# Kernel tuning notes

Hardware: AMD Instinct MI355X
Metric: run time of the kernel (lower is better)

## Reference

```python
import jax, jax.numpy as jnp
import numpy as np

NUM_EMBEDDINGS = 8192
EMBEDDING_DIM = 512
COMMITMENT_COST = 0.25
N_INPUTS = 32768


def setup_inputs() -> dict:
    key = jax.random.key(0)
    k1, k2 = jax.random.split(key)
    inputs = jax.random.normal(k1, (N_INPUTS, EMBEDDING_DIM), dtype=jnp.float32)
    weight = jax.random.normal(k2, (NUM_EMBEDDINGS, EMBEDDING_DIM), dtype=jnp.float32)
    return {"inputs": inputs, "weight": weight}


def reference(inputs, weight):
    # distances[n, k] = ||x_n||^2 + ||w_k||^2 - 2 x_n . w_k   -> [N, K]
    distances = (
        jnp.sum(inputs ** 2, axis=1, keepdims=True)
        + jnp.sum(weight ** 2, axis=1)
        - 2.0 * (inputs @ weight.T)
    )
    probs = jax.nn.softmax(-distances, axis=-1)            # [N, K]
    idx = jnp.argmin(distances, axis=1)                    # [N]
    quantized = weight[idx]                                # gather == one-hot @ weight

    e_latent_loss = jnp.mean((jax.lax.stop_gradient(quantized) - inputs) ** 2)
    q_latent_loss = jnp.mean((quantized - jax.lax.stop_gradient(inputs)) ** 2)
    loss = q_latent_loss + COMMITMENT_COST * e_latent_loss

    # straight-through estimator
    quantized_st = inputs + jax.lax.stop_gradient(quantized - inputs)

    # avg over one-hot encodings == normalized code histogram
    counts = jnp.bincount(idx, length=NUM_EMBEDDINGS).astype(inputs.dtype)
    avg_probs = counts / inputs.shape[0]
    perplexity = jnp.exp(-jnp.sum(avg_probs * jnp.log(avg_probs + 1e-10)))

    return (quantized_st, probs, loss, perplexity)
```

## Files before the change

### kernel.cpp

```cpp
#include <hip/hip_runtime.h>
#include <hip/hip_fp16.h>
#include <math.h>

#define N_ROWS 32768
#define K_CODES 8192
#define DIM 512

#define OUT_Q 0
#define OUT_P ((size_t)N_ROWS * DIM)
#define OUT_LOSS (OUT_P + (size_t)N_ROWS * K_CODES)
#define OUT_PERP (OUT_LOSS + 1)

#define WS_WSQ 0
#define WS_CNT (K_CODES)
#define WS_ERR (2 * K_CODES)
#define WS_RED (2 * K_CODES + N_ROWS)
#define WS_F16 (2 * K_CODES + N_ROWS + 64)

#define XH_OFF ((size_t)0)
#define XL_OFF ((size_t)N_ROWS * DIM)
#define WH_OFF ((size_t)2 * N_ROWS * DIM)
#define WL_OFF ((size_t)2 * N_ROWS * DIM + (size_t)K_CODES * DIM)
#define F16_COUNT ((size_t)2 * (N_ROWS + K_CODES) * DIM)
#define WS_NEEDED ((size_t)WS_F16 * 4 + F16_COUNT * 2)

typedef _Float16 f16x8 __attribute__((ext_vector_type(8)));
typedef float f32x4 __attribute__((ext_vector_type(4)));

__device__ inline void load_lds16(const void* g, void* l) {
    __builtin_amdgcn_global_load_lds((const __attribute__((address_space(1))) void*)g,
                                     (__attribute__((address_space(3))) void*)l,
                                     16, 0, 0);
}

__device__ inline unsigned int fkey(float f) {
    unsigned int b = __float_as_uint(f);
    return b ^ ((unsigned int)((int)b >> 31) | 0x80000000u);
}
__device__ inline float fkey_inv(unsigned int k) {
    unsigned int b = (k & 0x80000000u) ? (k ^ 0x80000000u) : ~k;
    return __uint_as_float(b);
}

__global__ void wsq_kernel(const float* __restrict__ W, float* __restrict__ ws) {
    int row = blockIdx.x;
    int lane = threadIdx.x;
    const float* src = W + (size_t)row * DIM;
    float4 v0 = *(const float4*)(src + lane * 8);
    float4 v1 = *(const float4*)(src + lane * 8 + 4);
    float s = v0.x * v0.x + v0.y * v0.y + v0.z * v0.z + v0.w * v0.w
            + v1.x * v1.x + v1.y * v1.y + v1.z * v1.z + v1.w * v1.w;
#pragma unroll
    for (int off = 32; off > 0; off >>= 1) s += __shfl_down(s, off, 64);
    if (lane == 0) ws[WS_WSQ + row] = s;
}

__global__ void __launch_bounds__(256) convert_split_kernel(
    const float* __restrict__ X, const float* __restrict__ W,
    _Float16* __restrict__ f16base, float* __restrict__ ws) {
    const size_t NX8 = (size_t)N_ROWS * DIM / 8;
    size_t t = (size_t)blockIdx.x * 256 + threadIdx.x;
    const float* src;
    _Float16 *hd, *ld;
    bool isW = (t >= NX8);
    if (!isW) {
        src = X + t * 8;
        hd = f16base + XH_OFF + t * 8;
        ld = f16base + XL_OFF + t * 8;
    } else {
        size_t u = t - NX8;
        src = W + u * 8;
        hd = f16base + WH_OFF + u * 8;
        ld = f16base + WL_OFF + u * 8;
    }
    float4 v0 = *(const float4*)src;
    float4 v1 = *(const float4*)(src + 4);
    float v[8] = {v0.x, v0.y, v0.z, v0.w, v1.x, v1.y, v1.z, v1.w};
    f16x8 h, l;
    float s = 0.f;
#pragma unroll
    for (int i = 0; i < 8; ++i) {
        _Float16 hv = (_Float16)v[i];
        h[i] = hv;
        l[i] = (_Float16)(v[i] - (float)hv);
        s += v[i] * v[i];
    }
    *(f16x8*)hd = h;
    *(f16x8*)ld = l;
    if (isW) {
#pragma unroll
        for (int off = 32; off > 0; off >>= 1) s += __shfl_down(s, off, 64);
        if ((threadIdx.x & 63) == 0) ws[WS_WSQ + ((t - NX8) >> 6)] = s;
    }
}

#define LDSB 24576
#define AH_O 0
#define AL_O 8192
#define BH_O 16384
#define BL_O 20480

__global__ void __launch_bounds__(512, 2) gemm_dist_mfma_kernel(
    const _Float16* __restrict__ f16base, const float* __restrict__ ws,
    float* __restrict__ out) {
    __shared__ _Float16 lds[3 * LDSB];

    const int tid = threadIdx.x;
    const int w = tid >> 6;
    const int lane = tid & 63;

    int lin = blockIdx.y * 64 + blockIdx.x;
    int xcd = lin & 7;
    int idx = lin >> 3;
    const int bn = (xcd * 8 + (idx & 7)) * 128;
    const int bm = (idx >> 3) * 256;

    const int wr = w >> 1;
    const int wc = w & 1;
    const int q = lane >> 4;
    const int fm = lane & 15;
    const int l4 = lane >> 2;
    const int p = lane & 3;

    f32x4 acc[4][4];
#pragma unroll
    for (int i = 0; i < 4; ++i)
#pragma unroll
        for (int j = 0; j < 4; ++j) acc[i][j] = (f32x4){0.f, 0.f, 0.f, 0.f};

    auto stage = [&](int ks, _Float16* buf, int part) {
        const int kk = ks * 32;
        int g = w * 2 + part;
        int arow = g * 16 + l4;
        int ca = p ^ ((arow >> 1) & 3);
        size_t aoff = (size_t)(bm + arow) * DIM + kk + ca * 8;
        load_lds16(f16base + XH_OFF + aoff, buf + AH_O + g * 512);
        load_lds16(f16base + XL_OFF + aoff, buf + AL_O + g * 512);
        int brow = w * 16 + l4;
        int cb = p ^ ((brow >> 1) & 3);
        size_t boff = (size_t)(bn + brow) * DIM + kk + cb * 8;
        if (part == 0)
            load_lds16(f16base + WH_OFF + boff, buf + BH_O + w * 512);
        else
            load_lds16(f16base + WL_OFF + boff, buf + BL_O + w * 512);
    };

    _Float16* c0 = lds;
    _Float16* c1 = lds + LDSB;
    _Float16* c2 = lds + 2 * LDSB;

    stage(0, c0, 0); stage(0, c0, 1);
    stage(1, c1, 0); stage(1, c1, 1);
    asm volatile("s_waitcnt vmcnt(6)" ::: "memory");
    __builtin_amdgcn_s_barrier();
    __builtin_amdgcn_sched_barrier(0);

#pragma unroll 1
    for (int ks = 0; ks < 16; ++ks) {
        if (ks < 14) { stage(ks + 2, c2, 0); stage(ks + 2, c2, 1); }

        f16x8 bhv[4], blv[4], ahv[4], alv[4];
#pragma unroll
        for (int j = 0; j < 4; ++j) {
            int bb = wc * 64 + j * 16 + fm;
            int off = bb * 32 + ((q ^ ((bb >> 1) & 3)) * 8);
            bhv[j] = *(const f16x8*)&c0[BH_O + off];
            blv[j] = *(const f16x8*)&c0[BL_O + off];
        }
#pragma unroll
        for (int i = 0; i < 4; ++i) {
            int am = wr * 64 + i * 16 + fm;
            int off = am * 32 + ((q ^ ((am >> 1) & 3)) * 8);
            ahv[i] = *(const f16x8*)&c0[AH_O + off];
            alv[i] = *(const f16x8*)&c0[AL_O + off];
        }

        __builtin_amdgcn_s_setprio(1);
#pragma unroll
        for (int i = 0; i < 4; ++i)
#pragma unroll
            for (int j = 0; j < 4; ++j) {
                acc[i][j] = __builtin_amdgcn_mfma_f32_16x16x32_f16(
                    ahv[i], bhv[j], acc[i][j], 0, 0, 0);
                acc[i][j] = __builtin_amdgcn_mfma_f32_16x16x32_f16(
                    ahv[i], blv[j], acc[i][j], 0, 0, 0);
                acc[i][j] = __builtin_amdgcn_mfma_f32_16x16x32_f16(
                    alv[i], bhv[j], acc[i][j], 0, 0, 0);
            }
        __builtin_amdgcn_s_setprio(0);

        if (ks < 14) {
            asm volatile("s_waitcnt vmcnt(6)" ::: "memory");
        } else if (ks == 14) {
            asm volatile("s_waitcnt vmcnt(0)" ::: "memory");
        }
        __builtin_amdgcn_s_barrier();
        __builtin_amdgcn_sched_barrier(0);

        _Float16* t0 = c0; c0 = c1; c1 = c2; c2 = t0;
    }

    const float* wsq = ws + WS_WSQ;
    float* Dout = out + OUT_P;
    const int q4 = q * 4;
#pragma unroll
    for (int i = 0; i < 4; ++i) {
#pragma unroll
        for (int j = 0; j < 4; ++j) {
            int n = bn + wc * 64 + j * 16 + fm;
            float wn = wsq[n];
#pragma unroll
            for (int r = 0; r < 4; ++r) {
                int m = bm + wr * 64 + i * 16 + q4 + r;
                Dout[(size_t)m * K_CODES + n] = wn - 2.f * acc[i][j][r];
            }
        }
    }
}

#define BM 128
#define BN 128
#define BK 16

__global__ void __launch_bounds__(256) gemm_dist_fp32_kernel(
    const float* __restrict__ X, const float* __restrict__ W,
    const float* __restrict__ ws, float* __restrict__ out) {
    __shared__ float As[BK][BM];
    __shared__ float Bs[BK][BN];

    const int bn = blockIdx.x * BN;
    const int bm = blockIdx.y * BM;
    const int tid = threadIdx.x;
    const int tx = tid & 15;
    const int ty = tid >> 4;
    const int lr = tid >> 1;
    const int lc = (tid & 1) * 8;

    float acc[8][8];
#pragma unroll
    for (int i = 0; i < 8; ++i)
#pragma unroll
        for (int j = 0; j < 8; ++j) acc[i][j] = 0.f;

    const float* aptr = X + (size_t)(bm + lr) * DIM + lc;
    const float* bptr = W + (size_t)(bn + lr) * DIM + lc;

    for (int k0 = 0; k0 < DIM; k0 += BK) {
        float4 a0 = *(const float4*)(aptr + k0);
        float4 a1 = *(const float4*)(aptr + k0 + 4);
        float4 b0 = *(const float4*)(bptr + k0);
        float4 b1 = *(const float4*)(bptr + k0 + 4);
        __syncthreads();
        As[lc + 0][lr] = a0.x; As[lc + 1][lr] = a0.y;
        As[lc + 2][lr] = a0.z; As[lc + 3][lr] = a0.w;
        As[lc + 4][lr] = a1.x; As[lc + 5][lr] = a1.y;
        As[lc + 6][lr] = a1.z; As[lc + 7][lr] = a1.w;
        Bs[lc + 0][lr] = b0.x; Bs[lc + 1][lr] = b0.y;
        Bs[lc + 2][lr] = b0.z; Bs[lc + 3][lr] = b0.w;
        Bs[lc + 4][lr] = b1.x; Bs[lc + 5][lr] = b1.y;
        Bs[lc + 6][lr] = b1.z; Bs[lc + 7][lr] = b1.w;
        __syncthreads();
#pragma unroll
        for (int kk = 0; kk < BK; ++kk) {
            float a[8], b[8];
            *(float4*)&a[0] = *(const float4*)&As[kk][ty * 8];
            *(float4*)&a[4] = *(const float4*)&As[kk][ty * 8 + 4];
            *(float4*)&b[0] = *(const float4*)&Bs[kk][tx * 8];
            *(float4*)&b[4] = *(const float4*)&Bs[kk][tx * 8 + 4];
#pragma unroll
            for (int i = 0; i < 8; ++i)
#pragma unroll
                for (int j = 0; j < 8; ++j)
                    acc[i][j] = fmaf(a[i], b[j], acc[i][j]);
        }
    }

    const float* wsq = ws + WS_WSQ;
    const int m0 = bm + ty * 8;
    const int n0 = bn + tx * 8;
    float wn[8];
    *(float4*)&wn[0] = *(const float4*)(wsq + n0);
    *(float4*)&wn[4] = *(const float4*)(wsq + n0 + 4);
    float* Dout = out + OUT_P;
#pragma unroll
    for (int i = 0; i < 8; ++i) {
        float4 o0, o1;
        o0.x = wn[0] - 2.f * acc[i][0];
        o0.y = wn[1] - 2.f * acc[i][1];
        o0.z = wn[2] - 2.f * acc[i][2];
        o0.w = wn[3] - 2.f * acc[i][3];
        o1.x = wn[4] - 2.f * acc[i][4];
        o1.y = wn[5] - 2.f * acc[i][5];
        o1.z = wn[6] - 2.f * acc[i][6];
        o1.w = wn[7] - 2.f * acc[i][7];
        float* drow = Dout + (size_t)(m0 + i) * K_CODES + n0;
        *(float4*)(drow) = o0;
        *(float4*)(drow + 4) = o1;
    }
}

__global__ void __launch_bounds__(512) probs_quant_kernel(
    const float* __restrict__ X, const float* __restrict__ W,
    float* __restrict__ out, float* __restrict__ ws) {
    const int n = blockIdx.x;
    const int tid = threadIdx.x;
    __shared__ unsigned long long mred[8];
    __shared__ float fred[8];

    float4* Drow4 = (float4*)(out + OUT_P + (size_t)n * K_CODES);

    const float x = X[(size_t)n * DIM + tid];

    float4 e[4];
    unsigned long long best = ~0ull;
#pragma unroll
    for (int t = 0; t < 4; ++t) {
        float4 v = Drow4[tid + t * 512];
        e[t] = v;
        unsigned int c0 = (unsigned int)((tid + t * 512) * 4);
        unsigned long long k;
        k = ((unsigned long long)fkey(v.x) << 32) | (c0 + 0u);
        best = k < best ? k : best;
        k = ((unsigned long long)fkey(v.y) << 32) | (c0 + 1u);
        best = k < best ? k : best;
        k = ((unsigned long long)fkey(v.z) << 32) | (c0 + 2u);
        best = k < best ? k : best;
        k = ((unsigned long long)fkey(v.w) << 32) | (c0 + 3u);
        best = k < best ? k : best;
    }
#pragma unroll
    for (int d = 1; d < 64; d <<= 1) {
        unsigned long long o = __shfl_xor(best, d, 64);
        best = o < best ? o : best;
    }
    if ((tid & 63) == 0) mred[tid >> 6] = best;
    __syncthreads();
    unsigned long long bm = mred[0];
#pragma unroll
    for (int i = 1; i < 8; ++i) bm = mred[i] < bm ? mred[i] : bm;
    const float smin = fkey_inv((unsigned int)(bm >> 32));
    const int amin = (int)(bm & 0xFFFFFFFFu);

    float sum = 0.f;
#pragma unroll
    for (int t = 0; t < 4; ++t) {
        float4 v = e[t];
        float4 ev;
        ev.x = __expf(smin - v.x);
        ev.y = __expf(smin - v.y);
        ev.z = __expf(smin - v.z);
        ev.w = __expf(smin - v.w);
        e[t] = ev;
        sum += ev.x + ev.y + ev.z + ev.w;
    }
#pragma unroll
    for (int off = 32; off > 0; off >>= 1) sum += __shfl_down(sum, off, 64);
    if ((tid & 63) == 0) fred[tid >> 6] = sum;
    __syncthreads();
    float tot = fred[0];
#pragma unroll
    for (int i = 1; i < 8; ++i) tot += fred[i];
    const float inv = 1.0f / tot;

#pragma unroll
    for (int t = 0; t < 4; ++t) {
        float4 ev = e[t];
        ev.x *= inv; ev.y *= inv; ev.z *= inv; ev.w *= inv;
        Drow4[tid + t * 512] = ev;
    }

    const float qv = W[(size_t)amin * DIM + tid];
    out[OUT_Q + (size_t)n * DIM + tid] = qv;
    float d2 = qv - x;
    float err = d2 * d2;
#pragma unroll
    for (int off = 32; off > 0; off >>= 1) err += __shfl_down(err, off, 64);
    __syncthreads();
    if ((tid & 63) == 0) fred[tid >> 6] = err;
    __syncthreads();
    if (tid == 0) {
        float e8 = fred[0];
#pragma unroll
        for (int i = 1; i < 8; ++i) e8 += fred[i];
        ws[WS_ERR + n] = e8;
        atomicAdd(ws + WS_CNT + amin, 1.0f);
    }
}

__global__ void __launch_bounds__(256) finalize_part_kernel(
    float* __restrict__ ws) {
    __shared__ float red[256];
    const int b = blockIdx.x;
    const int tid = threadIdx.x;

    float errsum = 0.f;
    const int ebase = b * 1024;
#pragma unroll
    for (int j = tid; j < 1024; j += 256) errsum += ws[WS_ERR + ebase + j];

    float p = ws[WS_CNT + b * 256 + tid] * (1.0f / (float)N_ROWS);
    float ent = -p * logf(p + 1e-10f);

    red[tid] = errsum;
    __syncthreads();
    for (int st = 128; st > 0; st >>= 1) {
        if (tid < st) red[tid] += red[tid + st];
        __syncthreads();
    }
    if (tid == 0) ws[WS_RED + b] = red[0];
    __syncthreads();
    red[tid] = ent;
    __syncthreads();
    for (int st = 128; st > 0; st >>= 1) {
        if (tid < st) red[tid] += red[tid + st];
        __syncthreads();
    }
    if (tid == 0) ws[WS_RED + 32 + b] = red[0];
}

__global__ void __launch_bounds__(64) finalize_fin_kernel(
    float* __restrict__ out, const float* __restrict__ ws) {
    const int tid = threadIdx.x;
    float ev = tid < 32 ? ws[WS_RED + tid] : 0.f;
    float nv = tid < 32 ? ws[WS_RED + 32 + tid] : 0.f;
#pragma unroll
    for (int off = 32; off > 0; off >>= 1) {
        ev += __shfl_down(ev, off, 64);
        nv += __shfl_down(nv, off, 64);
    }
    if (tid == 0) {
        float mse = ev * (1.0f / ((float)N_ROWS * (float)DIM));
        out[OUT_LOSS] = mse + 0.25f * mse;
        out[OUT_PERP] = expf(nv);
    }
}

extern "C" void kernel_launch(void* const* d_in, const int* in_sizes, int n_in,
                              void* d_out, int out_size, void* d_ws, size_t ws_size,
                              hipStream_t stream) {
    const float* X = (const float*)d_in[0];
    const float* W = (const float*)d_in[1];
    float* out = (float*)d_out;
    float* ws = (float*)d_ws;

    hipMemsetAsync(ws + WS_CNT, 0, K_CODES * sizeof(float), stream);

    if (ws_size >= WS_NEEDED) {
        _Float16* f16base = (_Float16*)(ws + WS_F16);
        const int conv_blocks =
            (int)(((size_t)(N_ROWS + K_CODES) * DIM / 8 + 255) / 256);
        convert_split_kernel<<<conv_blocks, 256, 0, stream>>>(X, W, f16base, ws);

        dim3 ggrid(64, 128);
        gemm_dist_mfma_kernel<<<ggrid, 512, 0, stream>>>(f16base, ws, out);
    } else {
        wsq_kernel<<<K_CODES, 64, 0, stream>>>(W, ws);
        dim3 ggrid(K_CODES / BN, N_ROWS / BM);
        gemm_dist_fp32_kernel<<<ggrid, 256, 0, stream>>>(X, W, ws, out);
    }

    probs_quant_kernel<<<N_ROWS, 512, 0, stream>>>(X, W, out, ws);
    finalize_part_kernel<<<32, 256, 0, stream>>>(ws);
    finalize_fin_kernel<<<1, 64, 0, stream>>>(out, ws);
}
```

Before: 2.349 ms.

## Fuse per-tile softmax max/sum and argmin into GEMM epilogue, add combine pass

```diff
diff --git a/kernel.cpp b/kernel.cpp
--- a/kernel.cpp
+++ b/kernel.cpp
@@ -15,17 +15,23 @@
 #define WS_CNT (K_CODES)
 #define WS_ERR (2 * K_CODES)
 #define WS_RED (2 * K_CODES + N_ROWS)
-#define WS_F16 (2 * K_CODES + N_ROWS + 64)
+#define WS_ROWMI (WS_RED + 64)
+#define WS_PSUM (WS_ROWMI + 2 * N_ROWS)
+#define WS_PMIN (WS_PSUM + (size_t)N_ROWS * 64)
+#define WS_F16_FULL (WS_PMIN + (size_t)2 * N_ROWS * 64)
+#define WS_F16_LEG  (WS_RED + 64)
 
 #define XH_OFF ((size_t)0)
 #define XL_OFF ((size_t)N_ROWS * DIM)
 #define WH_OFF ((size_t)2 * N_ROWS * DIM)
 #define WL_OFF ((size_t)2 * N_ROWS * DIM + (size_t)K_CODES * DIM)
 #define F16_COUNT ((size_t)2 * (N_ROWS + K_CODES) * DIM)
-#define WS_NEEDED ((size_t)WS_F16 * 4 + F16_COUNT * 2)
+#define NEEDED_FULL ((size_t)WS_F16_FULL * 4 + F16_COUNT * 2)
+#define NEEDED_LEG  ((size_t)WS_F16_LEG * 4 + F16_COUNT * 2)
 
 typedef _Float16 f16x8 __attribute__((ext_vector_type(8)));
 typedef float f32x4 __attribute__((ext_vector_type(4)));
+typedef unsigned long long u64;
 
 __device__ inline void load_lds16(const void* g, void* l) {
     __builtin_amdgcn_global_load_lds((const __attribute__((address_space(1))) void*)g,
@@ -102,8 +108,9 @@
 
 __global__ void __launch_bounds__(512, 2) gemm_dist_mfma_kernel(
     const _Float16* __restrict__ f16base, const float* __restrict__ ws,
-    float* __restrict__ out) {
-    __shared__ _Float16 lds[3 * LDSB];
+    float* __restrict__ out, u64* __restrict__ pmin_g,
+    float* __restrict__ psum_g) {
+    __shared__ __align__(16) _Float16 lds[3 * LDSB];
 
     const int tid = threadIdx.x;
     const int w = tid >> 6;
@@ -114,6 +121,7 @@
     int idx = lin >> 3;
     const int bn = (xcd * 8 + (idx & 7)) * 128;
     const int bm = (idx >> 3) * 256;
+    const int tile = bn >> 7;
 
     const int wr = w >> 1;
     const int wc = w & 1;
@@ -157,9 +165,7 @@
 
 #pragma unroll 1
     for (int ks = 0; ks < 16; ++ks) {
-        if (ks < 14) { stage(ks + 2, c2, 0); stage(ks + 2, c2, 1); }
-
-        f16x8 bhv[4], blv[4], ahv[4], alv[4];
+        f16x8 bhv[4], blv[4];
 #pragma unroll
         for (int j = 0; j < 4; ++j) {
             int bb = wc * 64 + j * 16 + fm;
@@ -167,28 +173,51 @@
             bhv[j] = *(const f16x8*)&c0[BH_O + off];
             blv[j] = *(const f16x8*)&c0[BL_O + off];
         }
-#pragma unroll
-        for (int i = 0; i < 4; ++i) {
+        f16x8 ah[2], al[2];
+#pragma unroll
+        for (int i = 0; i < 2; ++i) {
             int am = wr * 64 + i * 16 + fm;
             int off = am * 32 + ((q ^ ((am >> 1) & 3)) * 8);
-            ahv[i] = *(const f16x8*)&c0[AH_O + off];
-            alv[i] = *(const f16x8*)&c0[AL_O + off];
-        }
-
+            ah[i] = *(const f16x8*)&c0[AH_O + off];
+            al[i] = *(const f16x8*)&c0[AL_O + off];
+        }
+        if (ks < 14) stage(ks + 2, c2, 0);
         __builtin_amdgcn_s_setprio(1);
 #pragma unroll
-        for (int i = 0; i < 4; ++i)
+        for (int i = 0; i < 2; ++i)
 #pragma unroll
             for (int j = 0; j < 4; ++j) {
                 acc[i][j] = __builtin_amdgcn_mfma_f32_16x16x32_f16(
-                    ahv[i], bhv[j], acc[i][j], 0, 0, 0);
+                    ah[i], bhv[j], acc[i][j], 0, 0, 0);
                 acc[i][j] = __builtin_amdgcn_mfma_f32_16x16x32_f16(
-                    ahv[i], blv[j], acc[i][j], 0, 0, 0);
+                    ah[i], blv[j], acc[i][j], 0, 0, 0);
                 acc[i][j] = __builtin_amdgcn_mfma_f32_16x16x32_f16(
-                    alv[i], bhv[j], acc[i][j], 0, 0, 0);
+                    al[i], bhv[j], acc[i][j], 0, 0, 0);
             }
         __builtin_amdgcn_s_setprio(0);
-
+        __builtin_amdgcn_s_barrier();
+
+#pragma unroll
+        for (int i = 0; i < 2; ++i) {
+            int am = wr * 64 + (i + 2) * 16 + fm;
+            int off = am * 32 + ((q ^ ((am >> 1) & 3)) * 8);
+            ah[i] = *(const f16x8*)&c0[AH_O + off];
+            al[i] = *(const f16x8*)&c0[AL_O + off];
+        }
+        if (ks < 14) stage(ks + 2, c2, 1);
+        __builtin_amdgcn_s_setprio(1);
+#pragma unroll
+        for (int i = 0; i < 2; ++i)
+#pragma unroll
+            for (int j = 0; j < 4; ++j) {
+                acc[i + 2][j] = __builtin_amdgcn_mfma_f32_16x16x32_f16(
+                    ah[i], bhv[j], acc[i + 2][j], 0, 0, 0);
+                acc[i + 2][j] = __builtin_amdgcn_mfma_f32_16x16x32_f16(
+                    ah[i], blv[j], acc[i + 2][j], 0, 0, 0);
+                acc[i + 2][j] = __builtin_amdgcn_mfma_f32_16x16x32_f16(
+                    al[i], bhv[j], acc[i + 2][j], 0, 0, 0);
+            }
+        __builtin_amdgcn_s_setprio(0);
         if (ks < 14) {
             asm volatile("s_waitcnt vmcnt(6)" ::: "memory");
         } else if (ks == 14) {
@@ -203,18 +232,145 @@
     const float* wsq = ws + WS_WSQ;
     float* Dout = out + OUT_P;
     const int q4 = q * 4;
+    float wnj[4];
+#pragma unroll
+    for (int j = 0; j < 4; ++j) wnj[j] = wsq[bn + wc * 64 + j * 16 + fm];
+
 #pragma unroll
     for (int i = 0; i < 4; ++i) {
 #pragma unroll
         for (int j = 0; j < 4; ++j) {
             int n = bn + wc * 64 + j * 16 + fm;
-            float wn = wsq[n];
 #pragma unroll
             for (int r = 0; r < 4; ++r) {
                 int m = bm + wr * 64 + i * 16 + q4 + r;
-                Dout[(size_t)m * K_CODES + n] = wn - 2.f * acc[i][j][r];
+                Dout[(size_t)m * K_CODES + n] = wnj[j] - 2.f * acc[i][j][r];
             }
         }
+    }
+
+    if (pmin_g) {
+        u64* hmin = (u64*)lds;
+        float* hsum = (float*)(hmin + 512);
+
+#pragma unroll
+        for (int i = 0; i < 4; ++i) {
+#pragma unroll
+            for (int r = 0; r < 4; ++r) {
+                u64 bk = ~0ull;
+#pragma unroll
+                for (int j = 0; j < 4; ++j) {
+                    float S = wnj[j] - 2.f * acc[i][j][r];
+                    u64 kk = ((u64)fkey(S) << 32) |
+                             (unsigned int)(bn + wc * 64 + j * 16 + fm);
+                    bk = kk < bk ? kk : bk;
+                }
+#pragma unroll
+                for (int d = 1; d < 16; d <<= 1) {
+                    u64 o = __shfl_xor(bk, d, 64);
+                    bk = o < bk ? o : bk;
+                }
+                if (fm == 0) hmin[(wr * 64 + i * 16 + q4 + r) * 2 + wc] = bk;
+            }
+        }
+        __syncthreads();
+
+#pragma unroll
+        for (int i = 0; i < 4; ++i) {
+#pragma unroll
+            for (int r = 0; r < 4; ++r) {
+                int rl = wr * 64 + i * 16 + q4 + r;
+                u64 k0 = hmin[rl * 2 + 0], k1 = hmin[rl * 2 + 1];
+                u64 km = k1 < k0 ? k1 : k0;
+                float mt = fkey_inv((unsigned int)(km >> 32));
+                float s = 0.f;
+#pragma unroll
+                for (int j = 0; j < 4; ++j)
+                    s += __expf(mt - (wnj[j] - 2.f * acc[i][j][r]));
+#pragma unroll
+                for (int d = 1; d < 16; d <<= 1) s += __shfl_xor(s, d, 64);
+                if (fm == 0) hsum[rl * 2 + wc] = s;
+            }
+        }
+        __syncthreads();
+
+        if (wc == 0) {
+            int rl = wr * 64 + lane;
+            u64 k0 = hmin[rl * 2 + 0], k1 = hmin[rl * 2 + 1];
+            u64 km = k1 < k0 ? k1 : k0;
+            size_t o = (size_t)(bm + rl) * 64 + tile;
+            pmin_g[o] = km;
+            psum_g[o] = hsum[rl * 2 + 0] + hsum[rl * 2 + 1];
+        }
+    }
+}
+
+__global__ void __launch_bounds__(256) combine_kernel(
+    const float* __restrict__ X, const float* __restrict__ W,
+    float* __restrict__ out, float* __restrict__ ws) {
+    const int row = blockIdx.x * 4 + (threadIdx.x >> 6);
+    const int lane = threadIdx.x & 63;
+    const u64* pmin = (const u64*)(ws + WS_PMIN);
+    const float* psum = ws + WS_PSUM;
+
+    u64 k = pmin[(size_t)row * 64 + lane];
+    float s = psum[(size_t)row * 64 + lane];
+
+    u64 bk = k;
+#pragma unroll
+    for (int d = 1; d < 64; d <<= 1) {
+        u64 o = __shfl_xor(bk, d, 64);
+        bk = o < bk ? o : bk;
+    }
+    const float M = fkey_inv((unsigned int)(bk >> 32));
+    const int amin = (int)(bk & 0xFFFFFFFFu);
+
+    float t = __expf(M - fkey_inv((unsigned int)(k >> 32))) * s;
+#pragma unroll
+    for (int d = 1; d < 64; d <<= 1) t += __shfl_xor(t, d, 64);
+    const float inv = 1.0f / t;
+
+    if (lane == 0)
+        ((float2*)(ws + WS_ROWMI))[row] = make_float2(M, inv);
+
+    const float4* xr = (const float4*)(X + (size_t)row * DIM);
+    const float4* wr = (const float4*)(W + (size_t)amin * DIM);
+    float4* qr = (float4*)(out + OUT_Q + (size_t)row * DIM);
+    float err = 0.f;
+#pragma unroll
+    for (int t2 = 0; t2 < 2; ++t2) {
+        int i = lane + t2 * 64;
+        float4 xv = xr[i];
+        float4 wv = wr[i];
+        qr[i] = wv;
+        float dx = wv.x - xv.x, dy = wv.y - xv.y;
+        float dz = wv.z - xv.z, dw = wv.w - xv.w;
+        err += dx * dx + dy * dy + dz * dz + dw * dw;
+    }
+#pragma unroll
+    for (int d = 1; d < 64; d <<= 1) err += __shfl_xor(err, d, 64);
+    if (lane == 0) {
+        ws[WS_ERR + row] = err;
+        atomicAdd(ws + WS_CNT + amin, 1.0f);
+    }
+}
+
+__global__ void __launch_bounds__(256) ppass_kernel(
+    float* __restrict__ out, const float* __restrict__ ws) {
+    const float2* rowMI = (const float2*)(ws + WS_ROWMI);
+    float4* P = (float4*)(out + OUT_P);
+    const size_t total4 = (size_t)N_ROWS * K_CODES / 4;
+    const size_t stride = (size_t)gridDim.x * 256;
+    for (size_t i = (size_t)blockIdx.x * 256 + threadIdx.x; i < total4;
+         i += stride) {
+        int row = (int)(i >> 11);
+        float2 mi = rowMI[row];
+        float4 v = P[i];
+        v.x = __expf(mi.x - v.x) * mi.y;
+        v.y = __expf(mi.x - v.y) * mi.y;
+        v.z = __expf(mi.x - v.z) * mi.y;
+        v.w = __expf(mi.x - v.w) * mi.y;
+        P[i] = v;
     }
 }
 
@@ -308,7 +464,6 @@
     __shared__ float fred[8];
 
     float4* Drow4 = (float4*)(out + OUT_P + (size_t)n * K_CODES);
-
     const float x = X[(size_t)n * DIM + tid];
 
     float4 e[4];
@@ -445,21 +600,35 @@
 
     hipMemsetAsync(ws + WS_CNT, 0, K_CODES * sizeof(float), stream);
 
-    if (ws_size >= WS_NEEDED) {
-        _Float16* f16base = (_Float16*)(ws + WS_F16);
-        const int conv_blocks =
-            (int)(((size_t)(N_ROWS + K_CODES) * DIM / 8 + 255) / 256);
+    const int conv_blocks =
+        (int)(((size_t)(N_ROWS + K_CODES) * DIM / 8 + 255) / 256);
+
+    if (ws_size >= NEEDED_FULL) {
+        _Float16* f16base = (_Float16*)(ws + WS_F16_FULL);
         convert_split_kernel<<<conv_blocks, 256, 0, stream>>>(X, W, f16base, ws);
 
         dim3 ggrid(64, 128);
-        gemm_dist_mfma_kernel<<<ggrid, 512, 0, stream>>>(f16base, ws, out);
+        gemm_dist_mfma_kernel<<<ggrid, 512, 0, stream>>>(
+            f16base, ws, out, (u64*)(ws + WS_PMIN), ws + WS_PSUM);
+
+        combine_kernel<<<N_ROWS / 4, 256, 0, stream>>>(X, W, out, ws);
+        ppass_kernel<<<2048, 256, 0, stream>>>(out, ws);
+    } else if (ws_size >= NEEDED_LEG) {
+        _Float16* f16base = (_Float16*)(ws + WS_F16_LEG);
+        convert_split_kernel<<<conv_blocks, 256, 0, stream>>>(X, W, f16base, ws);
+
+        dim3 ggrid(64, 128);
+        gemm_dist_mfma_kernel<<<ggrid, 512, 0, stream>>>(
+            f16base, ws, out, nullptr, nullptr);
+
+        probs_quant_kernel<<<N_ROWS, 512, 0, stream>>>(X, W, out, ws);
     } else {
         wsq_kernel<<<K_CODES, 64, 0, stream>>>(W, ws);
         dim3 ggrid(K_CODES / BN, N_ROWS / BM);
         gemm_dist_fp32_kernel<<<ggrid, 256, 0, stream>>>(X, W, ws, out);
-    }
-
-    probs_quant_kernel<<<N_ROWS, 512, 0, stream>>>(X, W, out, ws);
+        probs_quant_kernel<<<N_ROWS, 512, 0, stream>>>(X, W, out, ws);
+    }
+
     finalize_part_kernel<<<32, 256, 0, stream>>>(ws);
     finalize_fin_kernel<<<1, 64, 0, stream>>>(out, ws);
 }
```

New measurement: 2.564 ms. 9.2% more time.
